# Kernel optimization log

Measured on AMD Instinct MI355X. Metric: run time of the kernel, lower is better.

The kernel has to match this reference:

```python
import jax, jax.numpy as jnp
import numpy as np

H_SIZE = 128
E_SIZE = 16
N_LAYERS = 3
N_ATOMS = 80000
N_BLOCKS = 16000
N_EDGES = 320000
N_GRAPHS = 128


def setup_inputs() -> dict:
    key = jax.random.key(0)
    ks = jax.random.split(key, 20)
    p = lambda k, shape: (0.02 * jax.random.normal(k, shape, dtype=jnp.float32))
    h = H_SIZE
    inp = {
        'H': jax.random.normal(ks[0], (N_ATOMS, h), dtype=jnp.float32),
        'Z': jax.random.normal(ks[1], (N_ATOMS, 1, 3), dtype=jnp.float32),
        'block_id': jnp.sort(jax.random.randint(ks[2], (N_ATOMS,), 0, N_BLOCKS)),
        'batch_id': jnp.sort(jax.random.randint(ks[3], (N_BLOCKS,), 0, N_GRAPHS)),
        'edges': jax.random.randint(ks[4], (2, N_EDGES), 0, N_BLOCKS),
        'edge_attr': jax.random.normal(ks[5], (N_EDGES, E_SIZE), dtype=jnp.float32),
        # EGNN parameters
        'emb_in_w': p(ks[6], (h, h)), 'emb_in_b': jnp.zeros((h,), jnp.float32),
        'emb_out_w': p(ks[7], (h, h)), 'emb_out_b': jnp.zeros((h,), jnp.float32),
        'edge_w1': p(ks[8], (N_LAYERS, 2 * h + 1 + E_SIZE, h)), 'edge_b1': jnp.zeros((N_LAYERS, h), jnp.float32),
        'edge_w2': p(ks[9], (N_LAYERS, h, h)), 'edge_b2': jnp.zeros((N_LAYERS, h), jnp.float32),
        'node_w1': p(ks[10], (N_LAYERS, 2 * h, h)), 'node_b1': jnp.zeros((N_LAYERS, h), jnp.float32),
        'node_w2': p(ks[11], (N_LAYERS, h, h)), 'node_b2': jnp.zeros((N_LAYERS, h), jnp.float32),
        'coord_w1': p(ks[12], (N_LAYERS, h, h)), 'coord_b1': jnp.zeros((N_LAYERS, h), jnp.float32),
        'coord_w3': p(ks[13], (N_LAYERS, h, 1)),  # final coord layer, no bias
    }
    return inp


def _normalize(x, eps=1e-12):
    # F.normalize(dim=-1): x / max(||x||_2, eps)
    n = jnp.linalg.norm(x, axis=-1, keepdims=True)
    return x / jnp.maximum(n, eps)


def _seg_mean(x, ids, n):
    s = jax.ops.segment_sum(x, ids, num_segments=n)
    c = jax.ops.segment_sum(jnp.ones((x.shape[0], 1), x.dtype), ids, num_segments=n)
    return s / jnp.maximum(c, 1.0)


def _egnn_forward(H, Z, block_id, batch_id, edges, edge_attr,
                  emb_in_w, emb_in_b, emb_out_w, emb_out_b,
                  edge_w1, edge_b1, edge_w2, edge_b2,
                  node_w1, node_b1, node_w2, node_b2,
                  coord_w1, coord_b1, coord_w3):
    silu = jax.nn.silu
    # atom -> block pooling (scatter_mean)
    Hm = _seg_mean(H, block_id, N_BLOCKS)                      # [B, h]
    x = _seg_mean(Z.reshape(Z.shape[0], -1), block_id, N_BLOCKS)  # [B, 3] (squeeze of [B,1,3])
    row, col = edges[0], edges[1]

    h = Hm @ emb_in_w + emb_in_b
    for l in range(N_LAYERS):
        diff = x[row] - x[col]                                 # [E, 3]
        radial = jnp.sum(diff * diff, axis=-1, keepdims=True)  # [E, 1]
        e_in = jnp.concatenate([h[row], h[col], radial, edge_attr], axis=-1)  # [E, 2h+1+e]
        m = silu(silu(e_in @ edge_w1[l] + edge_b1[l]) @ edge_w2[l] + edge_b2[l])  # edge MLP [E, h]
        # coordinate update: per-edge scalar weight, mean aggregation
        w = silu(m @ coord_w1[l] + coord_b1[l]) @ coord_w3[l]  # [E, 1]
        x = x + _seg_mean(diff * w, row, N_BLOCKS)
        # node update: sum aggregation of messages, residual
        agg = jax.ops.segment_sum(m, row, num_segments=N_BLOCKS)  # [B, h]
        h = h + (silu(jnp.concatenate([h, agg], axis=-1) @ node_w1[l] + node_b1[l]) @ node_w2[l] + node_b2[l])
    h = h @ emb_out_w + emb_out_b

    block_repr = _normalize(h)                                  # [B, h]
    graph_repr = _normalize(jax.ops.segment_sum(block_repr, batch_id, num_segments=N_GRAPHS))  # [G, h]
    return Hm, block_repr, graph_repr


def reference(H, Z, block_id, batch_id, edges, edge_attr,
              emb_in_w, emb_in_b, emb_out_w, emb_out_b,
              edge_w1, edge_b1, edge_w2, edge_b2,
              node_w1, node_b1, node_w2, node_b2,
              coord_w1, coord_b1, coord_w3):
    return _egnn_forward(H, Z, block_id, batch_id, edges, edge_attr,
                         emb_in_w, emb_in_b, emb_out_w, emb_out_b,
                         edge_w1, edge_b1, edge_w2, edge_b2,
                         node_w1, node_b1, node_w2, node_b2,
                         coord_w1, coord_b1, coord_w3)
```

## Files before the change

### kernel.cpp

```cpp
#include <hip/hip_runtime.h>

#define N_ATOMS  80000
#define N_BLOCKS 16000
#define N_EDGES  320000
#define N_GRAPHS 128
#define HS       128

typedef unsigned short ushortT;
typedef __attribute__((ext_vector_type(8))) __bf16 bf16x8;
typedef __attribute__((ext_vector_type(8))) unsigned short ushort8;
typedef __attribute__((ext_vector_type(4))) float f32x4;

__device__ __forceinline__ unsigned short f2bf(float f){
  unsigned int u = __builtin_bit_cast(unsigned int, f);
  u = (u + 0x7FFFu + ((u >> 16) & 1u)) >> 16;
  return (unsigned short)u;
}
__device__ __forceinline__ ushortT f2bff(float f){
  __bf16 b = (__bf16)f;
  return __builtin_bit_cast(ushortT, b);
}
__device__ __forceinline__ float bf2f(ushortT u){
  unsigned int v = ((unsigned int)u) << 16;
  return __builtin_bit_cast(float, v);
}
__device__ __forceinline__ bf16x8 load8bf(const ushortT* p){
  uint4 u = *reinterpret_cast<const uint4*>(p);
  return __builtin_bit_cast(bf16x8, u);
}
__device__ __forceinline__ bf16x8 load8f_bf(const float* p){
  float4 a = *reinterpret_cast<const float4*>(p);
  float4 b = *reinterpret_cast<const float4*>(p + 4);
  ushort8 u = { f2bff(a.x), f2bff(a.y), f2bff(a.z), f2bff(a.w),
                f2bff(b.x), f2bff(b.y), f2bff(b.z), f2bff(b.w) };
  return __builtin_bit_cast(bf16x8, u);
}
__device__ __forceinline__ float silu(float v){
  return v * __builtin_amdgcn_rcpf(1.f + __expf(-v));
}

__device__ __forceinline__ int c_of_p(int p){
  int ks = p >> 5, lg = (p >> 3) & 3, j = p & 7;
  return 16 * (ks * 2 + (j >> 2)) + lg * 4 + (j & 3);
}

__global__ void transpose_cvt_kernel(const float* __restrict__ src, ushortT* __restrict__ dst,
                                     int srcK, int row_off, int K, int N, int Kpad, int L,
                                     int perm_n, int perm_k){
  int idx = blockIdx.x * 256 + threadIdx.x;
  int tot = L * N * Kpad;
  if (idx >= tot) return;
  int k = idx % Kpad;
  int rem = idx / Kpad;
  int n = rem % N;
  int l = rem / N;
  float v = 0.f;
  if (k < K){
    int kk = perm_k ? c_of_p(k) : k;
    int nn = perm_n ? c_of_p(n) : n;
    v = src[((size_t)l * srcK + row_off + kk) * N + nn];
  }
  dst[idx] = f2bf(v);
}

__global__ void perm_bias_kernel(const float* __restrict__ src, float* __restrict__ dst, int L){
  int i = blockIdx.x * 256 + threadIdx.x;
  if (i >= L * 128) return;
  int l = i >> 7, p = i & 127;
  dst[i] = src[l * 128 + c_of_p(p)];
}

__global__ void block_start_kernel(const int* __restrict__ bid, int* __restrict__ start){
  int b = blockIdx.x * 256 + threadIdx.x;
  if (b > N_BLOCKS) return;
  int lo = 0, hi = N_ATOMS;
  while (lo < hi){ int mid = (lo + hi) >> 1; if (bid[mid] < b) lo = mid + 1; else hi = mid; }
  start[b] = lo;
}

__global__ void hist_kernel(const int* __restrict__ edges, int* __restrict__ hist){
  int e = blockIdx.x * 256 + threadIdx.x;
  if (e < N_EDGES) atomicAdd(&hist[edges[e]], 1);
}

__global__ void scan_kernel(const int* __restrict__ hist, int* __restrict__ estart,
                            int* __restrict__ ecur){
  __shared__ int ps[256];
  int t = threadIdx.x;
  const int chunk = (N_BLOCKS + 255) / 256;
  int lo = t * chunk, hi = lo + chunk;
  if (hi > N_BLOCKS) hi = N_BLOCKS;
  int s = 0;
  for (int i = lo; i < hi; i++) s += hist[i];
  ps[t] = s;
  __syncthreads();
  for (int off = 1; off < 256; off <<= 1){
    int v = (t >= off) ? ps[t - off] : 0;
    __syncthreads();
    ps[t] += v;
    __syncthreads();
  }
  int base = (t == 0) ? 0 : ps[t - 1];
  for (int i = lo; i < hi; i++){ estart[i] = base; ecur[i] = base; base += hist[i]; }
  if (t == 255) estart[N_BLOCKS] = base;
}

__global__ void scatter_kernel(const int* __restrict__ edges, const float* __restrict__ attr,
                               int* __restrict__ ecur,
                               int* __restrict__ srow, int* __restrict__ scol,
                               ushortT* __restrict__ sattr){
  int e = blockIdx.x * 256 + threadIdx.x;
  if (e >= N_EDGES) return;
  int r = edges[e], c = edges[N_EDGES + e];
  int p = atomicAdd(&ecur[r], 1);
  srow[p] = r; scol[p] = c;
  ushortT buf[32];
  buf[0] = 0;
#pragma unroll
  for (int k = 0; k < 16; k++) buf[k + 1] = f2bf(attr[(size_t)e * 16 + k]);
#pragma unroll
  for (int k = 17; k < 32; k++) buf[k] = 0;
#pragma unroll
  for (int k = 0; k < 16; k++)
    reinterpret_cast<uint*>(sattr + (size_t)p * 32)[k] = reinterpret_cast<uint*>(buf)[k];
}

__global__ void pool_kernel(const float* __restrict__ H, const float* __restrict__ Z,
                            const int* __restrict__ start,
                            float* __restrict__ Hm, float* __restrict__ x){
  int b = blockIdx.x;
  int t = threadIdx.x;
  int s = start[b], e = start[b + 1];
  float inv = 1.f / (float)((e - s) > 0 ? (e - s) : 1);
  float sum = 0.f;
  for (int a = s; a < e; a++) sum += H[(size_t)a * HS + t];
  Hm[(size_t)b * HS + t] = sum * inv;
  if (t < 3){
    float sz = 0.f;
    for (int a = s; a < e; a++) sz += Z[a * 3 + t];
    x[b * 3 + t] = sz * inv;
  }
}

__global__ __launch_bounds__(256) void gemm_pq_kernel(
    const float* __restrict__ A,
    const ushortT* __restrict__ Wt, const float* __restrict__ bias,
    float* __restrict__ Cf,
    const ushortT* __restrict__ Wa, const ushortT* __restrict__ Wb,
    const float* __restrict__ b1p,
    ushortT* __restrict__ Pbf, ushortT* __restrict__ Qbf,
    float* __restrict__ agg, float* __restrict__ xacc){
  __shared__ __align__(16) ushortT t1_s[4][2048];
  int t = threadIdx.x; int lane = t & 63; int wv = t >> 6;
  int l15 = lane & 15, lg = lane >> 4;
  int base = blockIdx.x * 64 + wv * 16;
  int row = base + l15;
  {
    float4 z4 = {0.f, 0.f, 0.f, 0.f};
    float4* aggp = reinterpret_cast<float4*>(agg + (size_t)blockIdx.x * 64 * HS);
#pragma unroll
    for (int i = 0; i < 8; i++) aggp[t + 256 * i] = z4;
    if (t < 192) xacc[blockIdx.x * 192 + t] = 0.f;
  }
  ushortT* T1 = t1_s[wv];
  f32x4 zero = {0.f, 0.f, 0.f, 0.f};
  f32x4 acc[8];
#pragma unroll
  for (int n = 0; n < 8; n++) acc[n] = zero;
#pragma unroll
  for (int ks = 0; ks < 4; ks++){
    int k0 = ks * 32 + lg * 8;
    bf16x8 af = load8f_bf(A + (size_t)row * HS + k0);
#pragma unroll
    for (int n = 0; n < 8; n++){
      bf16x8 bf = load8bf(Wt + (size_t)(16 * n + l15) * HS + k0);
      acc[n] = __builtin_amdgcn_mfma_f32_16x16x32_bf16(af, bf, acc[n], 0, 0, 0);
    }
  }
#pragma unroll
  for (int n = 0; n < 8; n++){
    int col = 16 * n + l15;
    float bv = bias[col];
#pragma unroll
    for (int r = 0; r < 4; r++){
      int ro = base + lg * 4 + r;
      int er = lg * 4 + r;
      float hv = acc[n][r] + bv;
      Cf[(size_t)ro * HS + col] = hv;
      T1[(er * 128 + col) ^ ((er & 7) << 3)] = f2bff(hv);
    }
  }
  f32x4 accp[8], accq[8];
#pragma unroll
  for (int n = 0; n < 8; n++){ accp[n] = zero; accq[n] = zero; }
#pragma unroll
  for (int ks = 0; ks < 4; ks++){
    int k0 = ks * 32 + lg * 8;
    bf16x8 af = load8bf(&T1[(l15 * 128 + k0) ^ ((l15 & 7) << 3)]);
#pragma unroll
    for (int n = 0; n < 8; n++){
      accp[n] = __builtin_amdgcn_mfma_f32_16x16x32_bf16(af, load8bf(Wa + (size_t)(16 * n + l15) * HS + k0), accp[n], 0, 0, 0);
      accq[n] = __builtin_amdgcn_mfma_f32_16x16x32_bf16(af, load8bf(Wb + (size_t)(16 * n + l15) * HS + k0), accq[n], 0, 0, 0);
    }
  }
#pragma unroll
  for (int n = 0; n < 8; n++){
    int col = 16 * n + l15;
    float bv = b1p[col];
#pragma unroll
    for (int r = 0; r < 4; r++){
      int ro = base + lg * 4 + r;
      Pbf[(size_t)ro * HS + col] = f2bff(accp[n][r] + bv);
      Qbf[(size_t)ro * HS + col] = f2bff(accq[n][r]);
    }
  }
}

template<bool PQ>
__global__ __launch_bounds__(256) void node_kernel(
    float* __restrict__ h, float* __restrict__ agg,
    const ushortT* __restrict__ W1t, const ushortT* __restrict__ W2t,
    const float* __restrict__ b1, const float* __restrict__ b2,
    const ushortT* __restrict__ Wa, const ushortT* __restrict__ Wb,
    const float* __restrict__ b1p,
    ushortT* __restrict__ Pbf, ushortT* __restrict__ Qbf,
    float* __restrict__ x, float* __restrict__ xacc, const int* __restrict__ estart){
  __shared__ __align__(16) ushortT t1_s[4][2048];
  int t = threadIdx.x; int lane = t & 63; int wv = t >> 6;
  int l15 = lane & 15, lg = lane >> 4;
  int base = blockIdx.x * 64 + wv * 16;
  int row = base + l15;
  ushortT* T1 = t1_s[wv];
  f32x4 zero = {0.f, 0.f, 0.f, 0.f};

  if (PQ){
    if (t < 192){
      int i = blockIdx.x * 192 + t;
      int b = i / 3;
      int cnt = estart[b + 1] - estart[b];
      x[i] += xacc[i] / (float)(cnt > 0 ? cnt : 1);
      xacc[i] = 0.f;
    }
  }

  f32x4 acc[8];
#pragma unroll
  for (int n = 0; n < 8; n++) acc[n] = zero;
#pragma unroll
  for (int ks = 0; ks < 8; ks++){
    int k0 = ks * 32 + lg * 8;
    bf16x8 af = (k0 < 128) ? load8f_bf(h + (size_t)row * HS + k0)
                           : load8f_bf(agg + (size_t)row * HS + (k0 - 128));
#pragma unroll
    for (int n = 0; n < 8; n++){
      acc[n] = __builtin_amdgcn_mfma_f32_16x16x32_bf16(af, load8bf(W1t + (size_t)(16 * n + l15) * 256 + k0), acc[n], 0, 0, 0);
    }
  }
  if (PQ){
    __syncthreads();
    float4 z4 = {0.f, 0.f, 0.f, 0.f};
    float4* aggp = reinterpret_cast<float4*>(agg + (size_t)blockIdx.x * 64 * HS);
#pragma unroll
    for (int i = 0; i < 8; i++) aggp[t + 256 * i] = z4;
  }
#pragma unroll
  for (int n = 0; n < 8; n++){
    int col = 16 * n + l15;
    float bv = b1[col];
#pragma unroll
    for (int r = 0; r < 4; r++){
      int er = lg * 4 + r;
      T1[(er * 128 + col) ^ ((er & 7) << 3)] = f2bff(silu(acc[n][r] + bv));
    }
  }
#pragma unroll
  for (int n = 0; n < 8; n++) acc[n] = zero;
#pragma unroll
  for (int ks = 0; ks < 4; ks++){
    int k0 = ks * 32 + lg * 8;
    bf16x8 af = load8bf(&T1[(l15 * 128 + k0) ^ ((l15 & 7) << 3)]);
#pragma unroll
    for (int n = 0; n < 8; n++){
      acc[n] = __builtin_amdgcn_mfma_f32_16x16x32_bf16(af, load8bf(W2t + (size_t)(16 * n + l15) * HS + k0), acc[n], 0, 0, 0);
    }
  }
#pragma unroll
  for (int n = 0; n < 8; n++){
    int col = 16 * n + l15;
    float bv = b2[col];
#pragma unroll
    for (int r = 0; r < 4; r++){
      int ro = base + lg * 4 + r;
      int er = lg * 4 + r;
      float hv = h[(size_t)ro * HS + col] + acc[n][r] + bv;
      h[(size_t)ro * HS + col] = hv;
      if (PQ) T1[(er * 128 + col) ^ ((er & 7) << 3)] = f2bff(hv);
    }
  }
  if (PQ){
    f32x4 accp[8], accq[8];
#pragma unroll
    for (int n = 0; n < 8; n++){ accp[n] = zero; accq[n] = zero; }
#pragma unroll
    for (int ks = 0; ks < 4; ks++){
      int k0 = ks * 32 + lg * 8;
      bf16x8 af = load8bf(&T1[(l15 * 128 + k0) ^ ((l15 & 7) << 3)]);
#pragma unroll
      for (int n = 0; n < 8; n++){
        accp[n] = __builtin_amdgcn_mfma_f32_16x16x32_bf16(af, load8bf(Wa + (size_t)(16 * n + l15) * HS + k0), accp[n], 0, 0, 0);
        accq[n] = __builtin_amdgcn_mfma_f32_16x16x32_bf16(af, load8bf(Wb + (size_t)(16 * n + l15) * HS + k0), accq[n], 0, 0, 0);
      }
    }
#pragma unroll
    for (int n = 0; n < 8; n++){
      int col = 16 * n + l15;
      float bv = b1p[col];
#pragma unroll
      for (int r = 0; r < 4; r++){
        int ro = base + lg * 4 + r;
        Pbf[(size_t)ro * HS + col] = f2bff(accp[n][r] + bv);
        Qbf[(size_t)ro * HS + col] = f2bff(accq[n][r]);
      }
    }
  }
}

__global__ __launch_bounds__(256) void emb_norm_kernel(
    const float* __restrict__ h, const ushortT* __restrict__ Wt,
    const float* __restrict__ bias, const int* __restrict__ batch_id,
    float* __restrict__ brep, float* __restrict__ gsum){
  int t = threadIdx.x; int lane = t & 63; int wv = t >> 6;
  int l15 = lane & 15, lg = lane >> 4;
  int base = blockIdx.x * 64 + wv * 16;
  int row = base + l15;
  f32x4 zero = {0.f, 0.f, 0.f, 0.f};
  f32x4 acc[8];
#pragma unroll
  for (int n = 0; n < 8; n++) acc[n] = zero;
#pragma unroll
  for (int ks = 0; ks < 4; ks++){
    int k0 = ks * 32 + lg * 8;
    bf16x8 af = load8f_bf(h + (size_t)row * HS + k0);
#pragma unroll
    for (int n = 0; n < 8; n++){
      acc[n] = __builtin_amdgcn_mfma_f32_16x16x32_bf16(af, load8bf(Wt + (size_t)(16 * n + l15) * HS + k0), acc[n], 0, 0, 0);
    }
  }
#pragma unroll
  for (int n = 0; n < 8; n++){
    float bv = bias[16 * n + l15];
#pragma unroll
    for (int r = 0; r < 4; r++) acc[n][r] += bv;
  }
  float scl[4];
#pragma unroll
  for (int r = 0; r < 4; r++){
    float ss = 0.f;
#pragma unroll
    for (int n = 0; n < 8; n++) ss += acc[n][r] * acc[n][r];
#pragma unroll
    for (int o = 1; o < 16; o <<= 1) ss += __shfl_xor(ss, o, 64);
    scl[r] = 1.f / fmaxf(sqrtf(ss), 1e-12f);
  }
#pragma unroll
  for (int r = 0; r < 4; r++){
    int ro = base + lg * 4 + r;
    int g = batch_id[ro];
#pragma unroll
    for (int n = 0; n < 8; n++){
      int col = 16 * n + l15;
      float v = acc[n][r] * scl[r];
      brep[(size_t)ro * HS + col] = v;
      atomicAdd(&gsum[g * HS + col], v);
    }
  }
}

template<int COORD>
__global__ __launch_bounds__(256, 4) void edge_kernel(
    const int* __restrict__ srow, const int* __restrict__ scol,
    const ushortT* __restrict__ sattr,
    const float* __restrict__ x,
    const ushortT* __restrict__ Pbf, const ushortT* __restrict__ Qbf,
    const ushortT* __restrict__ W1ct, const ushortT* __restrict__ W2tp,
    const ushortT* __restrict__ CW1tp,
    const float* __restrict__ b2, const float* __restrict__ cb1,
    const float* __restrict__ cw3,
    float* __restrict__ xacc, float* __restrict__ agg){
  __shared__ float bias_l[3][128];
  __shared__ int   rid_s[64];
  __shared__ float dif_s[COORD ? 64 : 1][3];
  __shared__ float wall[COORD ? 4 : 1][COORD ? 64 : 1];
  __shared__ __align__(16) ushortT S1[64 * 128];
  __shared__ __align__(16) ushortT S2[64 * 128];

  const int t = threadIdx.x;
  const int lane = t & 63;
  const int wv = t >> 6;
  const int l15 = lane & 15, lg = lane >> 4;
  const f32x4 zero = {0.f, 0.f, 0.f, 0.f};

  if (t < 128){
    bias_l[0][t] = b2[t];
    if (COORD){ bias_l[1][t] = cb1[t]; bias_l[2][t] = cw3[t]; }
  }

  const int erow = wv * 16 + l15;
  const int e = blockIdx.x * 64 + erow;
  const int r = srow[e], c = scol[e];
  const float dx = x[r * 3 + 0] - x[c * 3 + 0];
  const float dy = x[r * 3 + 1] - x[c * 3 + 1];
  const float dz = x[r * 3 + 2] - x[c * 3 + 2];
  const float rad = dx * dx + dy * dy + dz * dz;
  if (lg == 0){
    rid_s[erow] = r;
    if (COORD){ dif_s[erow][0] = dx; dif_s[erow][1] = dy; dif_s[erow][2] = dz; }
  }
  ushort8 at8 = __builtin_bit_cast(ushort8, load8bf(sattr + (size_t)e * 32 + lg * 8));
  if (lg == 0) at8[0] = f2bff(rad);
  const bf16x8 atb = __builtin_bit_cast(bf16x8, at8);

#pragma unroll
  for (int ks = 0; ks < 4; ks++){
    f32x4 a0 = __builtin_amdgcn_mfma_f32_16x16x32_bf16(
        load8bf(W1ct + (size_t)(16 * (2 * ks)     + l15) * 32 + lg * 8), atb, zero, 0, 0, 0);
    f32x4 a1 = __builtin_amdgcn_mfma_f32_16x16x32_bf16(
        load8bf(W1ct + (size_t)(16 * (2 * ks + 1) + l15) * 32 + lg * 8), atb, zero, 0, 0, 0);
    ushort8 pv = __builtin_bit_cast(ushort8, load8bf(Pbf + (size_t)r * HS + ks * 32 + lg * 8));
    ushort8 qv = __builtin_bit_cast(ushort8, load8bf(Qbf + (size_t)c * HS + ks * 32 + lg * 8));
    ushort8 af;
#pragma unroll
    for (int j = 0; j < 4; j++)
      af[j] = f2bff(silu(a0[j] + bf2f(pv[j]) + bf2f(qv[j])));
#pragma unroll
    for (int j = 4; j < 8; j++)
      af[j] = f2bff(silu(a1[j - 4] + bf2f(pv[j]) + bf2f(qv[j])));
    int byte = (erow * 256 + ks * 64 + lg * 16) ^ ((erow & 7) << 4);
    *reinterpret_cast<uint4*>(reinterpret_cast<char*>(S1) + byte) = __builtin_bit_cast(uint4, af);
  }
  __syncthreads();

  f32x4 acc2[4][2];
#pragma unroll
  for (int et = 0; et < 4; et++){ acc2[et][0] = zero; acc2[et][1] = zero; }
#pragma unroll
  for (int ks = 0; ks < 4; ks++){
    bf16x8 wf0 = load8bf(W2tp + (size_t)(16 * (2 * wv)     + l15) * HS + ks * 32 + lg * 8);
    bf16x8 wf1 = load8bf(W2tp + (size_t)(16 * (2 * wv + 1) + l15) * HS + ks * 32 + lg * 8);
#pragma unroll
    for (int et = 0; et < 4; et++){
      int row2 = et * 16 + l15;
      int byte = (row2 * 256 + ks * 64 + lg * 16) ^ ((row2 & 7) << 4);
      bf16x8 mb = __builtin_bit_cast(bf16x8,
          *reinterpret_cast<const uint4*>(reinterpret_cast<const char*>(S1) + byte));
      acc2[et][0] = __builtin_amdgcn_mfma_f32_16x16x32_bf16(wf0, mb, acc2[et][0], 0, 0, 0);
      acc2[et][1] = __builtin_amdgcn_mfma_f32_16x16x32_bf16(wf1, mb, acc2[et][1], 0, 0, 0);
    }
  }
#pragma unroll
  for (int g = 0; g < 2; g++){
    int n = 2 * wv + g;
    float4 bv = *reinterpret_cast<const float4*>(&bias_l[0][16 * n + lg * 4]);
    int pbyte = ((n >> 1) * 32 + lg * 8 + (n & 1) * 4) * 2;
#pragma unroll
    for (int et = 0; et < 4; et++){
      ushortT mm[4];
#pragma unroll
      for (int rr = 0; rr < 4; rr++)
        mm[rr] = f2bff(silu(acc2[et][g][rr] + (&bv.x)[rr]));
      int row2 = et * 16 + l15;
      int byte = (row2 * 256 + pbyte) ^ ((row2 & 7) << 4);
      *reinterpret_cast<uint2*>(reinterpret_cast<char*>(S2) + byte) =
          *reinterpret_cast<uint2*>(mm);
    }
  }
  __syncthreads();

  if (COORD){
    f32x4 acc3[4][2];
#pragma unroll
    for (int et = 0; et < 4; et++){ acc3[et][0] = zero; acc3[et][1] = zero; }
#pragma unroll
    for (int ks = 0; ks < 4; ks++){
      bf16x8 wf0 = load8bf(CW1tp + (size_t)(16 * (2 * wv)     + l15) * HS + ks * 32 + lg * 8);
      bf16x8 wf1 = load8bf(CW1tp + (size_t)(16 * (2 * wv + 1) + l15) * HS + ks * 32 + lg * 8);
#pragma unroll
      for (int et = 0; et < 4; et++){
        int row2 = et * 16 + l15;
        int byte = (row2 * 256 + ks * 64 + lg * 16) ^ ((row2 & 7) << 4);
        bf16x8 mb = __builtin_bit_cast(bf16x8,
            *reinterpret_cast<const uint4*>(reinterpret_cast<const char*>(S2) + byte));
        acc3[et][0] = __builtin_amdgcn_mfma_f32_16x16x32_bf16(wf0, mb, acc3[et][0], 0, 0, 0);
        acc3[et][1] = __builtin_amdgcn_mfma_f32_16x16x32_bf16(wf1, mb, acc3[et][1], 0, 0, 0);
      }
    }
#pragma unroll
    for (int et = 0; et < 4; et++){
      float ws = 0.f;
#pragma unroll
      for (int g = 0; g < 2; g++){
        int n = 2 * wv + g;
        float4 cbv = *reinterpret_cast<const float4*>(&bias_l[1][16 * n + lg * 4]);
        float4 cwv = *reinterpret_cast<const float4*>(&bias_l[2][16 * n + lg * 4]);
#pragma unroll
        for (int rr = 0; rr < 4; rr++)
          ws += silu(acc3[et][g][rr] + (&cbv.x)[rr]) * (&cwv.x)[rr];
      }
      ws += __shfl_xor(ws, 16, 64);
      ws += __shfl_xor(ws, 32, 64);
      if (lg == 0) wall[wv][et * 16 + l15] = ws;
    }
  }

  {
    const int c0 = c_of_p(2 * lane), c1 = c_of_p(2 * lane + 1);
    float run0 = 0.f, run1 = 0.f;
    int prev = __builtin_amdgcn_readfirstlane(rid_s[wv * 16]);
#pragma unroll
    for (int e2 = 0; e2 < 16; e2++){
      int re = __builtin_amdgcn_readfirstlane(rid_s[wv * 16 + e2]);
      if (re != prev){
        atomicAdd(&agg[(size_t)prev * HS + c0], run0);
        atomicAdd(&agg[(size_t)prev * HS + c1], run1);
        run0 = 0.f; run1 = 0.f; prev = re;
      }
      int row2 = wv * 16 + e2;
      int byte = (row2 * 256 + lane * 4) ^ ((row2 & 7) << 4);
      uint u = *reinterpret_cast<const uint*>(reinterpret_cast<const char*>(S2) + byte);
      run0 += bf2f((ushortT)(u & 0xFFFF));
      run1 += bf2f((ushortT)(u >> 16));
    }
    atomicAdd(&agg[(size_t)prev * HS + c0], run0);
    atomicAdd(&agg[(size_t)prev * HS + c1], run1);
  }

  if (COORD){
    __syncthreads();
    if (t < 192){
      int e2 = t / 3, cd = t % 3;
      float w = wall[0][e2] + wall[1][e2] + wall[2][e2] + wall[3][e2];
      atomicAdd(&xacc[(size_t)rid_s[e2] * 3 + cd], dif_s[e2][cd] * w);
    }
  }
}

__global__ void norm_graph_kernel(const float* __restrict__ gsum, float* __restrict__ grep){
  int wv = threadIdx.x >> 6, lane = threadIdx.x & 63;
  int g = blockIdx.x * 4 + wv;
  if (g >= N_GRAPHS) return;
  float v0 = gsum[g * HS + lane];
  float v1 = gsum[g * HS + 64 + lane];
  float ss = v0 * v0 + v1 * v1;
#pragma unroll
  for (int o = 1; o < 64; o <<= 1) ss += __shfl_xor(ss, o, 64);
  float s = 1.f / fmaxf(sqrtf(ss), 1e-12f);
  grep[(size_t)g * HS + lane] = v0 * s;
  grep[(size_t)g * HS + 64 + lane] = v1 * s;
}

extern "C" void kernel_launch(void* const* d_in, const int* in_sizes, int n_in,
                              void* d_out, int out_size, void* d_ws, size_t ws_size,
                              hipStream_t stream){
  const float* H         = (const float*)d_in[0];
  const float* Z         = (const float*)d_in[1];
  const int*   block_id  = (const int*)d_in[2];
  const int*   batch_id  = (const int*)d_in[3];
  const int*   edges     = (const int*)d_in[4];
  const float* edge_attr = (const float*)d_in[5];
  const float* emb_in_w  = (const float*)d_in[6];
  const float* emb_in_b  = (const float*)d_in[7];
  const float* emb_out_w = (const float*)d_in[8];
  const float* emb_out_b = (const float*)d_in[9];
  const float* edge_w1   = (const float*)d_in[10];
  const float* edge_b1   = (const float*)d_in[11];
  const float* edge_w2   = (const float*)d_in[12];
  const float* edge_b2   = (const float*)d_in[13];
  const float* node_w1   = (const float*)d_in[14];
  const float* node_b1   = (const float*)d_in[15];
  const float* node_w2   = (const float*)d_in[16];
  const float* node_b2   = (const float*)d_in[17];
  const float* coord_w1  = (const float*)d_in[18];
  const float* coord_b1  = (const float*)d_in[19];
  const float* coord_w3  = (const float*)d_in[20];

  float* out  = (float*)d_out;
  float* Hm   = out;
  float* brep = out + (size_t)N_BLOCKS * HS;
  float* grep = out + (size_t)2 * N_BLOCKS * HS;

  char* base = (char*)d_ws;
  size_t off = 0;
  auto take = [&](size_t bytes) -> char* {
    char* p = base + off;
    off += (bytes + 255) & ~(size_t)255;
    return p;
  };
  float*   x     = (float*)  take((size_t)N_BLOCKS * 3 * 4);
  float*   xacc  = (float*)  take((size_t)N_BLOCKS * 3 * 4);
  float*   h     = (float*)  take((size_t)N_BLOCKS * HS * 4);
  float*   agg   = (float*)  take((size_t)N_BLOCKS * HS * 4);
  float*   gsum  = (float*)  take((size_t)N_GRAPHS * HS * 4);
  int*     bstart= (int*)    take((size_t)(N_BLOCKS + 1) * 4);
  int*     hist  = (int*)    take((size_t)N_BLOCKS * 4);
  int*     estart= (int*)    take((size_t)(N_BLOCKS + 1) * 4);
  int*     ecur  = (int*)    take((size_t)N_BLOCKS * 4);
  int*     srow  = (int*)    take((size_t)N_EDGES * 4);
  int*     scol  = (int*)    take((size_t)N_EDGES * 4);
  ushortT* sattr = (ushortT*)take((size_t)N_EDGES * 32 * 2);
  ushortT* Pbf   = (ushortT*)take((size_t)N_BLOCKS * HS * 2);
  ushortT* Qbf   = (ushortT*)take((size_t)N_BLOCKS * HS * 2);
  ushortT* W1atp = (ushortT*)take((size_t)3 * 128 * 128 * 2);
  ushortT* W1btp = (ushortT*)take((size_t)3 * 128 * 128 * 2);
  ushortT* W1ct  = (ushortT*)take((size_t)3 * 128 * 32 * 2);
  ushortT* W2tp  = (ushortT*)take((size_t)3 * 128 * 128 * 2);
  ushortT* CW1tp = (ushortT*)take((size_t)3 * 128 * 128 * 2);
  ushortT* NW1t  = (ushortT*)take((size_t)3 * 128 * 256 * 2);
  ushortT* NW2t  = (ushortT*)take((size_t)3 * 128 * 128 * 2);
  ushortT* Eint  = (ushortT*)take((size_t)128 * 128 * 2);
  ushortT* Eoutt = (ushortT*)take((size_t)128 * 128 * 2);
  float*   b1p   = (float*)  take((size_t)3 * 128 * 4);

  transpose_cvt_kernel<<<(3*128*128 + 255)/256, 256, 0, stream>>>(edge_w1, W1atp, 273,   0, 128, 128, 128, 3, 1, 0);
  transpose_cvt_kernel<<<(3*128*128 + 255)/256, 256, 0, stream>>>(edge_w1, W1btp, 273, 128, 128, 128, 128, 3, 1, 0);
  transpose_cvt_kernel<<<(3*128*32  + 255)/256, 256, 0, stream>>>(edge_w1, W1ct,  273, 256,  17, 128,  32, 3, 0, 0);
  transpose_cvt_kernel<<<(3*128*128 + 255)/256, 256, 0, stream>>>(edge_w2, W2tp,  128,   0, 128, 128, 128, 3, 0, 1);
  transpose_cvt_kernel<<<(3*128*128 + 255)/256, 256, 0, stream>>>(coord_w1, CW1tp,128,   0, 128, 128, 128, 3, 0, 1);
  transpose_cvt_kernel<<<(3*128*256 + 255)/256, 256, 0, stream>>>(node_w1, NW1t,  256,   0, 256, 128, 256, 3, 0, 0);
  transpose_cvt_kernel<<<(3*128*128 + 255)/256, 256, 0, stream>>>(node_w2, NW2t,  128,   0, 128, 128, 128, 3, 0, 0);
  transpose_cvt_kernel<<<(128*128 + 255)/256, 256, 0, stream>>>(emb_in_w,  Eint,  128,   0, 128, 128, 128, 1, 0, 0);
  transpose_cvt_kernel<<<(128*128 + 255)/256, 256, 0, stream>>>(emb_out_w, Eoutt, 128,   0, 128, 128, 128, 1, 0, 0);
  perm_bias_kernel<<<2, 256, 0, stream>>>(edge_b1, b1p, 3);

  hipMemsetAsync(hist, 0, (size_t)N_BLOCKS * 4, stream);
  hist_kernel<<<N_EDGES / 256, 256, 0, stream>>>(edges, hist);
  scan_kernel<<<1, 256, 0, stream>>>(hist, estart, ecur);
  scatter_kernel<<<N_EDGES / 256, 256, 0, stream>>>(edges, edge_attr, ecur, srow, scol, sattr);

  block_start_kernel<<<(N_BLOCKS + 1 + 255) / 256, 256, 0, stream>>>(block_id, bstart);
  pool_kernel<<<N_BLOCKS, 128, 0, stream>>>(H, Z, bstart, Hm, x);

  gemm_pq_kernel<<<N_BLOCKS / 64, 256, 0, stream>>>(Hm, Eint, emb_in_b, h,
                                                    W1atp, W1btp, b1p, Pbf, Qbf, agg, xacc);

  for (int l = 0; l < 3; l++){
    if (l < 2){
      edge_kernel<1><<<N_EDGES / 64, 256, 0, stream>>>(
          srow, scol, sattr, x, Pbf, Qbf,
          W1ct + (size_t)l * 128 * 32, W2tp + (size_t)l * 128 * 128, CW1tp + (size_t)l * 128 * 128,
          edge_b2 + l * 128, coord_b1 + l * 128, coord_w3 + l * 128,
          xacc, agg);
      node_kernel<true><<<N_BLOCKS / 64, 256, 0, stream>>>(
          h, agg, NW1t + (size_t)l * 128 * 256, NW2t + (size_t)l * 128 * 128,
          node_b1 + l * 128, node_b2 + l * 128,
          W1atp + (size_t)(l + 1) * 128 * 128, W1btp + (size_t)(l + 1) * 128 * 128,
          b1p + (l + 1) * 128, Pbf, Qbf, x, xacc, estart);
    } else {
      edge_kernel<0><<<N_EDGES / 64, 256, 0, stream>>>(
          srow, scol, sattr, x, Pbf, Qbf,
          W1ct + (size_t)l * 128 * 32, W2tp + (size_t)l * 128 * 128, CW1tp + (size_t)l * 128 * 128,
          edge_b2 + l * 128, coord_b1 + l * 128, coord_w3 + l * 128,
          xacc, agg);
      node_kernel<false><<<N_BLOCKS / 64, 256, 0, stream>>>(
          h, agg, NW1t + (size_t)l * 128 * 256, NW2t + (size_t)l * 128 * 128,
          node_b1 + l * 128, node_b2 + l * 128,
          nullptr, nullptr, nullptr, nullptr, nullptr, nullptr, nullptr, nullptr);
    }
  }

  hipMemsetAsync(gsum, 0, (size_t)N_GRAPHS * HS * 4, stream);
  emb_norm_kernel<<<N_BLOCKS / 64, 256, 0, stream>>>(h, Eoutt, emb_out_b, batch_id, brep, gsum);
  norm_graph_kernel<<<N_GRAPHS / 4, 256, 0, stream>>>(gsum, grep);
}
```

Baseline: 558.4 us.

## Merge prep launches and memsets, drop edge-kernel shared staging

Merges the nine weight transpose/convert launches, the bias permutation and the hist memset into one prep kernel. It also fuses the edge histogram with the block-start search, and moves the gsum zeroing into the pool kernel. This cuts about a dozen small launches and two memsets, each of which adds fixed overhead. In the edge kernel, bias values are now read straight from global memory, row ids come via wave shuffles, and the wall scratch reuses the S1 buffer. This reduces LDS footprint and the staging writes, possibly raising occupancy, at the cost of more global bias loads.

```diff
diff --git a/kernel.cpp b/kernel.cpp
--- a/kernel.cpp
+++ b/kernel.cpp
@@ -44,43 +44,73 @@
   return 16 * (ks * 2 + (j >> 2)) + lg * 4 + (j & 3);
 }
 
-__global__ void transpose_cvt_kernel(const float* __restrict__ src, ushortT* __restrict__ dst,
-                                     int srcK, int row_off, int K, int N, int Kpad, int L,
-                                     int perm_n, int perm_k){
-  int idx = blockIdx.x * 256 + threadIdx.x;
-  int tot = L * N * Kpad;
-  if (idx >= tot) return;
+struct PrepParams {
+  const float* ew1; const float* ew2; const float* cw1;
+  const float* nw1; const float* nw2; const float* ei; const float* eo;
+  const float* eb1;
+  ushortT* W1atp; ushortT* W1btp; ushortT* W1ct; ushortT* W2tp; ushortT* CW1tp;
+  ushortT* NW1t; ushortT* NW2t; ushortT* Eint; ushortT* Eoutt;
+  float* b1p; int* hist;
+};
+
+__device__ __forceinline__ void tcvt(int idx, const float* __restrict__ src,
+                                     ushortT* __restrict__ dst,
+                                     int srcK, int row_off, int K, int N, int Kpad,
+                                     int pn, int pk){
   int k = idx % Kpad;
   int rem = idx / Kpad;
   int n = rem % N;
   int l = rem / N;
   float v = 0.f;
   if (k < K){
-    int kk = perm_k ? c_of_p(k) : k;
-    int nn = perm_n ? c_of_p(n) : n;
+    int kk = pk ? c_of_p(k) : k;
+    int nn = pn ? c_of_p(n) : n;
     v = src[((size_t)l * srcK + row_off + kk) * N + nn];
   }
   dst[idx] = f2bf(v);
 }
 
-__global__ void perm_bias_kernel(const float* __restrict__ src, float* __restrict__ dst, int L){
-  int i = blockIdx.x * 256 + threadIdx.x;
-  if (i >= L * 128) return;
-  int l = i >> 7, p = i & 127;
-  dst[i] = src[l * 128 + c_of_p(p)];
-}
-
-__global__ void block_start_kernel(const int* __restrict__ bid, int* __restrict__ start){
-  int b = blockIdx.x * 256 + threadIdx.x;
-  if (b > N_BLOCKS) return;
-  int lo = 0, hi = N_ATOMS;
-  while (lo < hi){ int mid = (lo + hi) >> 1; if (bid[mid] < b) lo = mid + 1; else hi = mid; }
-  start[b] = lo;
-}
-
-__global__ void hist_kernel(const int* __restrict__ edges, int* __restrict__ hist){
-  int e = blockIdx.x * 256 + threadIdx.x;
-  if (e < N_EDGES) atomicAdd(&hist[edges[e]], 1);
+#define PREP_TOTAL (49152*5 + 12288 + 98304 + 16384*2 + 16000 + 384)
+
+__global__ void prep_kernel(PrepParams P){
+  int idx = blockIdx.x * 256 + threadIdx.x;
+  if (idx < 49152){ tcvt(idx, P.ew1, P.W1atp, 273,   0, 128, 128, 128, 1, 0); return; }
+  idx -= 49152;
+  if (idx < 49152){ tcvt(idx, P.ew1, P.W1btp, 273, 128, 128, 128, 128, 1, 0); return; }
+  idx -= 49152;
+  if (idx < 12288){ tcvt(idx, P.ew1, P.W1ct,  273, 256,  17, 128,  32, 0, 0); return; }
+  idx -= 12288;
+  if (idx < 49152){ tcvt(idx, P.ew2, P.W2tp,  128,   0, 128, 128, 128, 0, 1); return; }
+  idx -= 49152;
+  if (idx < 49152){ tcvt(idx, P.cw1, P.CW1tp, 128,   0, 128, 128, 128, 0, 1); return; }
+  idx -= 49152;
+  if (idx < 98304){ tcvt(idx, P.nw1, P.NW1t,  256,   0, 256, 128, 256, 0, 0); return; }
+  idx -= 98304;
+  if (idx < 49152){ tcvt(idx, P.nw2, P.NW2t,  128,   0, 128, 128, 128, 0, 0); return; }
+  idx -= 49152;
+  if (idx < 16384){ tcvt(idx, P.ei,  P.Eint,  128,   0, 128, 128, 128, 0, 0); return; }
+  idx -= 16384;
+  if (idx < 16384){ tcvt(idx, P.eo,  P.Eoutt, 128,   0, 128, 128, 128, 0, 0); return; }
+  idx -= 16384;
+  if (idx < 16000){ P.hist[idx] = 0; return; }
+  idx -= 16000;
+  if (idx < 384){ int l = idx >> 7, p = idx & 127; P.b1p[idx] = P.eb1[l * 128 + c_of_p(p)]; }
+}
+
+__global__ void hist_bstart_kernel(const int* __restrict__ edges, int* __restrict__ hist,
+                                   const int* __restrict__ bid, int* __restrict__ bstart){
+  int b = blockIdx.x;
+  if (b < N_EDGES / 256){
+    int e = b * 256 + threadIdx.x;
+    atomicAdd(&hist[edges[e]], 1);
+  } else {
+    int i = (b - N_EDGES / 256) * 256 + threadIdx.x;
+    if (i <= N_BLOCKS){
+      int lo = 0, hi = N_ATOMS;
+      while (lo < hi){ int mid = (lo + hi) >> 1; if (bid[mid] < i) lo = mid + 1; else hi = mid; }
+      bstart[i] = lo;
+    }
+  }
 }
 
 __global__ void scan_kernel(const int* __restrict__ hist, int* __restrict__ estart,
@@ -127,9 +157,11 @@
 
 __global__ void pool_kernel(const float* __restrict__ H, const float* __restrict__ Z,
                             const int* __restrict__ start,
-                            float* __restrict__ Hm, float* __restrict__ x){
+                            float* __restrict__ Hm, float* __restrict__ x,
+                            float* __restrict__ gsum){
   int b = blockIdx.x;
   int t = threadIdx.x;
+  if (b < 128) gsum[b * 128 + t] = 0.f;
   int s = start[b], e = start[b + 1];
   float inv = 1.f / (float)((e - s) > 0 ? (e - s) : 1);
   float sum = 0.f;
@@ -387,23 +419,15 @@
     const float* __restrict__ b2, const float* __restrict__ cb1,
     const float* __restrict__ cw3,
     float* __restrict__ xacc, float* __restrict__ agg){
-  __shared__ float bias_l[3][128];
-  __shared__ int   rid_s[64];
-  __shared__ float dif_s[COORD ? 64 : 1][3];
-  __shared__ float wall[COORD ? 4 : 1][COORD ? 64 : 1];
   __shared__ __align__(16) ushortT S1[64 * 128];
   __shared__ __align__(16) ushortT S2[64 * 128];
+  float* wall = reinterpret_cast<float*>(S1);
 
   const int t = threadIdx.x;
   const int lane = t & 63;
   const int wv = t >> 6;
   const int l15 = lane & 15, lg = lane >> 4;
   const f32x4 zero = {0.f, 0.f, 0.f, 0.f};
-
-  if (t < 128){
-    bias_l[0][t] = b2[t];
-    if (COORD){ bias_l[1][t] = cb1[t]; bias_l[2][t] = cw3[t]; }
-  }
 
   const int erow = wv * 16 + l15;
   const int e = blockIdx.x * 64 + erow;
@@ -412,10 +436,6 @@
   const float dy = x[r * 3 + 1] - x[c * 3 + 1];
   const float dz = x[r * 3 + 2] - x[c * 3 + 2];
   const float rad = dx * dx + dy * dy + dz * dz;
-  if (lg == 0){
-    rid_s[erow] = r;
-    if (COORD){ dif_s[erow][0] = dx; dif_s[erow][1] = dy; dif_s[erow][2] = dz; }
-  }
   ushort8 at8 = __builtin_bit_cast(ushort8, load8bf(sattr + (size_t)e * 32 + lg * 8));
   if (lg == 0) at8[0] = f2bff(rad);
   const bf16x8 atb = __builtin_bit_cast(bf16x8, at8);
@@ -460,7 +480,7 @@
 #pragma unroll
   for (int g = 0; g < 2; g++){
     int n = 2 * wv + g;
-    float4 bv = *reinterpret_cast<const float4*>(&bias_l[0][16 * n + lg * 4]);
+    float4 bv = *reinterpret_cast<const float4*>(b2 + 16 * n + lg * 4);
     int pbyte = ((n >> 1) * 32 + lg * 8 + (n & 1) * 4) * 2;
 #pragma unroll
     for (int et = 0; et < 4; et++){
@@ -500,25 +520,25 @@
 #pragma unroll
       for (int g = 0; g < 2; g++){
         int n = 2 * wv + g;
-        float4 cbv = *reinterpret_cast<const float4*>(&bias_l[1][16 * n + lg * 4]);
-        float4 cwv = *reinterpret_cast<const float4*>(&bias_l[2][16 * n + lg * 4]);
+        float4 cbv = *reinterpret_cast<const float4*>(cb1 + 16 * n + lg * 4);
+        float4 cwv = *reinterpret_cast<const float4*>(cw3 + 16 * n + lg * 4);
 #pragma unroll
         for (int rr = 0; rr < 4; rr++)
           ws += silu(acc3[et][g][rr] + (&cbv.x)[rr]) * (&cwv.x)[rr];
       }
       ws += __shfl_xor(ws, 16, 64);
       ws += __shfl_xor(ws, 32, 64);
-      if (lg == 0) wall[wv][et * 16 + l15] = ws;
+      if (lg == 0) wall[wv * 64 + et * 16 + l15] = ws;
     }
   }
 
   {
     const int c0 = c_of_p(2 * lane), c1 = c_of_p(2 * lane + 1);
     float run0 = 0.f, run1 = 0.f;
-    int prev = __builtin_amdgcn_readfirstlane(rid_s[wv * 16]);
+    int prev = __builtin_amdgcn_readfirstlane(__shfl(r, 0, 64));
 #pragma unroll
     for (int e2 = 0; e2 < 16; e2++){
-      int re = __builtin_amdgcn_readfirstlane(rid_s[wv * 16 + e2]);
+      int re = __builtin_amdgcn_readfirstlane(__shfl(r, e2, 64));
       if (re != prev){
         atomicAdd(&agg[(size_t)prev * HS + c0], run0);
         atomicAdd(&agg[(size_t)prev * HS + c1], run1);
@@ -536,10 +556,10 @@
 
   if (COORD){
     __syncthreads();
-    if (t < 192){
-      int e2 = t / 3, cd = t % 3;
-      float w = wall[0][e2] + wall[1][e2] + wall[2][e2] + wall[3][e2];
-      atomicAdd(&xacc[(size_t)rid_s[e2] * 3 + cd], dif_s[e2][cd] * w);
+    float w = wall[erow] + wall[64 + erow] + wall[128 + erow] + wall[192 + erow];
+    if (lg < 3){
+      float d = (lg == 0) ? dx : ((lg == 1) ? dy : dz);
+      atomicAdd(&xacc[(size_t)r * 3 + lg], d * w);
     }
   }
 }
@@ -620,24 +640,20 @@
   ushortT* Eoutt = (ushortT*)take((size_t)128 * 128 * 2);
   float*   b1p   = (float*)  take((size_t)3 * 128 * 4);
 
-  transpose_cvt_kernel<<<(3*128*128 + 255)/256, 256, 0, stream>>>(edge_w1, W1atp, 273,   0, 128, 128, 128, 3, 1, 0);
-  transpose_cvt_kernel<<<(3*128*128 + 255)/256, 256, 0, stream>>>(edge_w1, W1btp, 273, 128, 128, 128, 128, 3, 1, 0);
-  transpose_cvt_kernel<<<(3*128*32  + 255)/256, 256, 0, stream>>>(edge_w1, W1ct,  273, 256,  17, 128,  32, 3, 0, 0);
-  transpose_cvt_kernel<<<(3*128*128 + 255)/256, 256, 0, stream>>>(edge_w2, W2tp,  128,   0, 128, 128, 128, 3, 0, 1);
-  transpose_cvt_kernel<<<(3*128*128 + 255)/256, 256, 0, stream>>>(coord_w1, CW1tp,128,   0, 128, 128, 128, 3, 0, 1);
-  transpose_cvt_kernel<<<(3*128*256 + 255)/256, 256, 0, stream>>>(node_w1, NW1t,  256,   0, 256, 128, 256, 3, 0, 0);
-  transpose_cvt_kernel<<<(3*128*128 + 255)/256, 256, 0, stream>>>(node_w2, NW2t,  128,   0, 128, 128, 128, 3, 0, 0);
-  transpose_cvt_kernel<<<(128*128 + 255)/256, 256, 0, stream>>>(emb_in_w,  Eint,  128,   0, 128, 128, 128, 1, 0, 0);
-  transpose_cvt_kernel<<<(128*128 + 255)/256, 256, 0, stream>>>(emb_out_w, Eoutt, 128,   0, 128, 128, 128, 1, 0, 0);
-  perm_bias_kernel<<<2, 256, 0, stream>>>(edge_b1, b1p, 3);
-
-  hipMemsetAsync(hist, 0, (size_t)N_BLOCKS * 4, stream);
-  hist_kernel<<<N_EDGES / 256, 256, 0, stream>>>(edges, hist);
+  PrepParams P;
+  P.ew1 = edge_w1; P.ew2 = edge_w2; P.cw1 = coord_w1;
+  P.nw1 = node_w1; P.nw2 = node_w2; P.ei = emb_in_w; P.eo = emb_out_w;
+  P.eb1 = edge_b1;
+  P.W1atp = W1atp; P.W1btp = W1btp; P.W1ct = W1ct; P.W2tp = W2tp; P.CW1tp = CW1tp;
+  P.NW1t = NW1t; P.NW2t = NW2t; P.Eint = Eint; P.Eoutt = Eoutt;
+  P.b1p = b1p; P.hist = hist;
+  prep_kernel<<<(PREP_TOTAL + 255) / 256, 256, 0, stream>>>(P);
+
+  hist_bstart_kernel<<<N_EDGES / 256 + (N_BLOCKS + 1 + 255) / 256, 256, 0, stream>>>(
+      edges, hist, block_id, bstart);
   scan_kernel<<<1, 256, 0, stream>>>(hist, estart, ecur);
   scatter_kernel<<<N_EDGES / 256, 256, 0, stream>>>(edges, edge_attr, ecur, srow, scol, sattr);
-
-  block_start_kernel<<<(N_BLOCKS + 1 + 255) / 256, 256, 0, stream>>>(block_id, bstart);
-  pool_kernel<<<N_BLOCKS, 128, 0, stream>>>(H, Z, bstart, Hm, x);
+  pool_kernel<<<N_BLOCKS, 128, 0, stream>>>(H, Z, bstart, Hm, x, gsum);
 
   gemm_pq_kernel<<<N_BLOCKS / 64, 256, 0, stream>>>(Hm, Eint, emb_in_b, h,
                                                     W1atp, W1btp, b1p, Pbf, Qbf, agg, xacc);
@@ -667,7 +683,6 @@
     }
   }
 
-  hipMemsetAsync(gsum, 0, (size_t)N_GRAPHS * HS * 4, stream);
   emb_norm_kernel<<<N_BLOCKS / 64, 256, 0, stream>>>(h, Eoutt, emb_out_b, batch_id, brep, gsum);
   norm_graph_kernel<<<N_GRAPHS / 4, 256, 0, stream>>>(gsum, grep);
 }
```

New measurement: 596.9 us. 1.07x slower.
